# Kernel optimization log

Measured on AMD Instinct MI355X. Metric: run time of the kernel, lower is better.

The kernel has to match this reference:

```python
import jax, jax.numpy as jnp
import numpy as np

N_NODES = 100_000
N_EDGES = 1_600_000
HID = 64
LAYERS = 3
MAX_ATOM = 100
BATCH = 16


def setup_inputs() -> dict:
    key = jax.random.key(0)
    ks = jax.random.split(key, 24)
    s = 0.05  # weight scale
    inp = {
        "x": jax.random.normal(ks[0], (N_NODES, 3), dtype=jnp.float32),
        "z": jax.random.randint(ks[1], (N_NODES,), 0, MAX_ATOM),
        "t": jax.random.uniform(ks[2], (BATCH, 1), dtype=jnp.float32),
        "edge_index": jax.random.randint(ks[3], (2, N_EDGES), 0, N_NODES),
        # atom embedding table
        "emb": jax.random.normal(ks[4], (MAX_ATOM, HID)) * s,
        # time embedding MLP: Linear(1,H), SiLU, Linear(H,H)
        "t_w1": jax.random.normal(ks[5], (1, HID)) * s,
        "t_b1": jnp.zeros((HID,)),
        "t_w2": jax.random.normal(ks[6], (HID, HID)) * s,
        "t_b2": jnp.zeros((HID,)),
        # per-layer EGNN params, stacked over layers
        # edge MLP: Linear(2H+1, H), SiLU, Linear(H, H), SiLU
        "e_w1": jax.random.normal(ks[7], (LAYERS, 2 * HID + 1, HID)) * s,
        "e_b1": jnp.zeros((LAYERS, HID)),
        "e_w2": jax.random.normal(ks[8], (LAYERS, HID, HID)) * s,
        "e_b2": jnp.zeros((LAYERS, HID)),
        # coord MLP: Linear(H, H), SiLU, Linear(H, 1)
        "c_w1": jax.random.normal(ks[9], (LAYERS, HID, HID)) * s,
        "c_b1": jnp.zeros((LAYERS, HID)),
        "c_w2": jax.random.normal(ks[10], (LAYERS, HID, 1)) * s,
        "c_b2": jnp.zeros((LAYERS, 1)),
        # node MLP: Linear(2H, H), SiLU, Linear(H, H), residual
        "n_w1": jax.random.normal(ks[11], (LAYERS, 2 * HID, HID)) * s,
        "n_b1": jnp.zeros((LAYERS, HID)),
        "n_w2": jax.random.normal(ks[12], (LAYERS, HID, HID)) * s,
        "n_b2": jnp.zeros((LAYERS, HID)),
    }
    return inp


def reference(x, z, t, edge_index, emb,
              t_w1, t_b1, t_w2, t_b2,
              e_w1, e_b1, e_w2, e_b2,
              c_w1, c_b1, c_w2, c_b2,
              n_w1, n_b1, n_w2, n_b2):
    silu = jax.nn.silu
    n = x.shape[0]
    # atom embedding + global time conditioning
    h = emb[z]                                           # (N, H)
    t_emb = silu(t @ t_w1 + t_b1) @ t_w2 + t_b2          # (B, H)
    h = h + jnp.mean(t_emb, axis=0, keepdims=True)
    src, dst = edge_index[0], edge_index[1]
    for l in range(LAYERS):
        diff = x[dst] - x[src]                           # (E, 3)
        d2 = jnp.sum(diff * diff, axis=-1, keepdims=True)  # (E, 1)
        ef = jnp.concatenate([h[dst], h[src], d2], axis=-1)  # (E, 2H+1)
        m = silu(silu(ef @ e_w1[l] + e_b1[l]) @ e_w2[l] + e_b2[l])  # (E, H)
        cw = silu(m @ c_w1[l] + c_b1[l]) @ c_w2[l] + c_b2[l]        # (E, 1)
        x = x + jax.ops.segment_sum(diff * cw, dst, num_segments=n)
        agg = jax.ops.segment_sum(m, dst, num_segments=n)           # (N, H)
        nf = jnp.concatenate([h, agg], axis=-1)                     # (N, 2H)
        h = h + (silu(nf @ n_w1[l] + n_b1[l]) @ n_w2[l] + n_b2[l])
    return x
```

## Files before the change

kernel.cpp:

```cpp
#include <hip/hip_runtime.h>

typedef __attribute__((ext_vector_type(8))) short s8v;
typedef __attribute__((ext_vector_type(4))) float f32x4;

#define MFMA16(A,B,C) __builtin_amdgcn_mfma_f32_16x16x32_bf16((A),(B),(C),0,0,0)

__device__ __forceinline__ float b2f(unsigned short s){
  union { unsigned u; float f; } v; v.u = ((unsigned)s) << 16; return v.f;
}
__device__ __forceinline__ unsigned short f2b(float f){
  union { float f; unsigned u; } v; v.f = f;
  return (unsigned short)((v.u + 0x8000u) >> 16);
}
__device__ __forceinline__ float siluf(float x){
  return x * __builtin_amdgcn_rcpf(1.f + __expf(-x));
}


__global__ void hist_kernel(const int* __restrict__ dst, int* __restrict__ deg, int E){
  int i = blockIdx.x*256 + threadIdx.x;
  if (i < E) atomicAdd(&deg[dst[i]], 1);
}

__global__ void scan1_kernel(const int* __restrict__ deg, int* __restrict__ rp,
                             int* __restrict__ bsum, int N){
  __shared__ int s[256];
  const int base = blockIdx.x*1024;
  const int t = threadIdx.x;
  int v[4];
  #pragma unroll
  for (int j = 0; j < 4; ++j){
    int idx = base + t*4 + j;
    v[j] = (idx < N) ? deg[idx] : 0;
  }
  const int tsum = v[0]+v[1]+v[2]+v[3];
  s[t] = tsum;
  __syncthreads();
  for (int off = 1; off < 256; off <<= 1){
    int x = (t >= off) ? s[t-off] : 0;
    __syncthreads();
    s[t] += x;
    __syncthreads();
  }
  const int incl = s[t];
  if (t == 255) bsum[blockIdx.x] = incl;
  int run = incl - tsum;
  #pragma unroll
  for (int j = 0; j < 4; ++j){
    int idx = base + t*4 + j;
    if (idx < N) rp[idx] = run;
    run += v[j];
  }
}

__global__ void scan2_kernel(int* __restrict__ bsum, int nb){
  __shared__ int s[256];
  const int t = threadIdx.x;
  const int v = (t < nb) ? bsum[t] : 0;
  s[t] = v;
  __syncthreads();
  for (int off = 1; off < 256; off <<= 1){
    int x = (t >= off) ? s[t-off] : 0;
    __syncthreads();
    s[t] += x;
    __syncthreads();
  }
  if (t < nb) bsum[t] = s[t] - v;
}

__global__ void scan3_kernel(int* __restrict__ rp, const int* __restrict__ bsum,
                             int N, int E){
  int i = blockIdx.x*256 + threadIdx.x;
  if (i < N) rp[i] += bsum[i >> 10];
  if (i == 0) rp[N] = E;
}

__global__ void scatter_kernel(const int* __restrict__ src, const int* __restrict__ dst,
                               const int* __restrict__ rp, int* __restrict__ cursor,
                               int* __restrict__ csr_src, int E){
  int i = blockIdx.x*256 + threadIdx.x;
  if (i < E){
    const int d = dst[i];
    const int pos = rp[d] + atomicAdd(&cursor[d], 1);
    csr_src[pos] = src[i];
  }
}


__global__ void tmean_kernel(const float* __restrict__ t,
                             const float* __restrict__ tw1,
                             const float* __restrict__ tb1,
                             const float* __restrict__ tw2,
                             const float* __restrict__ tb2,
                             float* __restrict__ tmean){
  __shared__ __align__(16) float s1[16*64];
  int j = threadIdx.x;
  float w1 = tw1[j], bb1 = tb1[j];
  for (int b = 0; b < 16; ++b)
    s1[b*64 + j] = siluf(t[b] * w1 + bb1);
  __syncthreads();
  float acc = 0.f;
  for (int b = 0; b < 16; ++b)
    for (int k = 0; k < 64; ++k)
      acc += s1[b*64 + k] * tw2[k*64 + j];
  tmean[j] = tb2[j] + acc * (1.f/16.f);
}

__global__ void init_h_kernel(const int* __restrict__ z,
                              const float* __restrict__ emb,
                              const float* __restrict__ tmean,
                              float* __restrict__ hf,
                              unsigned short* __restrict__ hb, int N){
  int i = blockIdx.x*256 + threadIdx.x;
  if (i >= N*64) return;
  int j = i & 63;
  int n = i >> 6;
  float v = emb[z[n]*64 + j] + tmean[j];
  hf[i] = v;
  hb[i] = f2b(v);
}


__global__ __launch_bounds__(512) void p12_kernel(
    const unsigned short* __restrict__ hb,
    const float* __restrict__ ew1, const float* __restrict__ eb1,
    unsigned short* __restrict__ P1, unsigned short* __restrict__ P2,
    int layer, int N)
{
  __shared__ __align__(16) short w1a[64*72];
  __shared__ __align__(16) short w1b[64*72];
  __shared__ __align__(16) float b1s[64];

  const int tid = threadIdx.x;
  const float* w1g = ew1 + layer*129*64;
  for (int idx = tid; idx < 64*64; idx += 512){
    int k = idx >> 6, n = idx & 63;
    w1a[n*72 + k] = (short)f2b(w1g[k*64 + n]);
    w1b[n*72 + k] = (short)f2b(w1g[(64 + k)*64 + n]);
  }
  if (tid < 64) b1s[tid] = eb1[layer*64 + tid];
  __syncthreads();

  const int lane = tid & 63;
  const int wv = tid >> 6;
  const int q = lane >> 4;
  const int n16 = lane & 15;

  const int ntile = N >> 4;
  const int step = gridDim.x * 8;
  for (int t = blockIdx.x*8 + wv; t < ntile; t += step){
    const int row = t*16 + n16;
    const s8v* ph = (const s8v*)(hb + row*64);
    const s8v a0 = ph[q];
    const s8v a1 = ph[4+q];
    #pragma unroll
    for (int nt = 0; nt < 4; ++nt){
      const s8v* wa = (const s8v*)&w1a[(nt*16 + n16)*72];
      const s8v* wb = (const s8v*)&w1b[(nt*16 + n16)*72];
      f32x4 aA = {0.f,0.f,0.f,0.f};
      aA = MFMA16(a0, wa[q],   aA);
      aA = MFMA16(a1, wa[4+q], aA);
      f32x4 aB = {0.f,0.f,0.f,0.f};
      aB = MFMA16(a0, wb[q],   aB);
      aB = MFMA16(a1, wb[4+q], aB);
      const float bb = b1s[nt*16 + n16];
      #pragma unroll
      for (int r = 0; r < 4; ++r){
        const int o = (t*16 + q*4 + r)*64 + nt*16 + n16;
        P1[o] = f2b(aA[r] + bb);
        P2[o] = f2b(aB[r]);
      }
    }
  }
}


__global__ __launch_bounds__(512) void edge_csr_kernel(
    const int* __restrict__ rp, const int* __restrict__ csr_src,
    const float* __restrict__ x_in, float* __restrict__ x_out,
    const unsigned short* __restrict__ P1, const unsigned short* __restrict__ P2,
    unsigned short* __restrict__ aggb,
    const float* __restrict__ ew1,
    const float* __restrict__ ew2, const float* __restrict__ eb2,
    const float* __restrict__ cw1, const float* __restrict__ cb1,
    const float* __restrict__ cw2, const float* __restrict__ cb2,
    int layer, int do_agg, int N)
{
  __shared__ __align__(16) short wT2[64*72];
  __shared__ __align__(16) short wc1T[64*72];
  __shared__ __align__(16) short sc[8][16*72];
  __shared__ __align__(16) float sdiff[8][48];

  const int tid = threadIdx.x;
  const float* w2g = ew2 + layer*64*64;
  const float* c1g = cw1 + layer*64*64;
  for (int idx = tid; idx < 64*64; idx += 512){
    int k = idx >> 6, n = idx & 63;
    wT2[n*72 + k]  = (short)f2b(w2g[k*64 + n]);
    wc1T[n*72 + k] = (short)f2b(c1g[k*64 + n]);
  }

  const int lane = tid & 63;
  const int wv = tid >> 6;
  const int q = lane >> 4;
  const int n16 = lane & 15;
  short* mysc = sc[wv];
  float* mydiff = sdiff[wv];

  const float* wlg = ew1 + layer*129*64 + 128*64;
  float wl_lo[8], wl_hi[8];
  #pragma unroll
  for (int j = 0; j < 8; ++j){
    wl_lo[j] = wlg[q*8 + j];
    wl_hi[j] = wlg[32 + q*8 + j];
  }
  float be2r[4], bc1r[4], cw2r[4];
  #pragma unroll
  for (int nt = 0; nt < 4; ++nt){
    be2r[nt] = eb2[layer*64 + nt*16 + n16];
    bc1r[nt] = cb1[layer*64 + nt*16 + n16];
    cw2r[nt] = cw2[layer*64 + nt*16 + n16];
  }
  const float cb2s = cb2[layer];
  __syncthreads();

  const int nwave = gridDim.x * 8;
  for (int n = blockIdx.x*8 + wv; n < N; n += nwave){
    const int start = rp[n];
    const int deg = rp[n+1] - start;

    const s8v* pd = (const s8v*)(P1 + (size_t)n*64);
    const s8v lo1 = pd[q];
    const s8v hi1 = pd[4+q];
    const float xd0 = x_in[n*3+0];
    const float xd1 = x_in[n*3+1];
    const float xd2 = x_in[n*3+2];

    float colsum[4] = {0.f,0.f,0.f,0.f};
    float xacc0 = 0.f, xacc1 = 0.f, xacc2 = 0.f;

    const int nch = (deg + 15) >> 4;
    for (int c = 0; c < nch; ++c){
      const int row = c*16 + n16;
      const int si = (row < deg) ? csr_src[start + row] : n;
      const float xs0 = x_in[si*3+0];
      const float xs1 = x_in[si*3+1];
      const float xs2 = x_in[si*3+2];
      const float dx = xd0 - xs0;
      const float dy = xd1 - xs1;
      const float dz = xd2 - xs2;
      const float d2 = dx*dx + dy*dy + dz*dz;
      if (q == 0){ mydiff[n16*3+0]=dx; mydiff[n16*3+1]=dy; mydiff[n16*3+2]=dz; }

      const s8v* ps = (const s8v*)(P2 + (size_t)si*64);
      const s8v lo2 = ps[q];
      const s8v hi2 = ps[4+q];

      s8v alo, ahi;
      #pragma unroll
      for (int j = 0; j < 8; ++j){
        const float v0 = b2f((unsigned short)lo1[j]) + b2f((unsigned short)lo2[j]) + d2*wl_lo[j];
        alo[j] = (short)f2b(siluf(v0));
        const float v1 = b2f((unsigned short)hi1[j]) + b2f((unsigned short)hi2[j]) + d2*wl_hi[j];
        ahi[j] = (short)f2b(siluf(v1));
      }

      f32x4 acc2[4];
      #pragma unroll
      for (int nt = 0; nt < 4; ++nt){
        const s8v* wb = (const s8v*)&wT2[(nt*16 + n16)*72];
        f32x4 a = {0.f,0.f,0.f,0.f};
        a = MFMA16(alo, wb[q],   a);
        a = MFMA16(ahi, wb[4+q], a);
        acc2[nt] = a;
      }
      const int rowbase = c*16 + q*4;
      #pragma unroll
      for (int nt = 0; nt < 4; ++nt){
        const float bb = be2r[nt];
        #pragma unroll
        for (int r = 0; r < 4; ++r){
          const float mv = siluf(acc2[nt][r] + bb);
          mysc[(q*4 + r)*72 + nt*16 + n16] = (short)f2b(mv);
          colsum[nt] += (rowbase + r < deg) ? mv : 0.f;
        }
      }
      __builtin_amdgcn_wave_barrier();
      const s8v* srd = (const s8v*)&mysc[n16*72];
      const s8v m0 = srd[q];
      const s8v m1 = srd[4+q];
      __builtin_amdgcn_wave_barrier();

      float pr[4] = {0.f,0.f,0.f,0.f};
      #pragma unroll
      for (int nt = 0; nt < 4; ++nt){
        const s8v* wb = (const s8v*)&wc1T[(nt*16 + n16)*72];
        f32x4 a = {0.f,0.f,0.f,0.f};
        a = MFMA16(m0, wb[q],   a);
        a = MFMA16(m1, wb[4+q], a);
        const float bc = bc1r[nt];
        const float wc2 = cw2r[nt];
        #pragma unroll
        for (int r = 0; r < 4; ++r) pr[r] += siluf(a[r] + bc) * wc2;
      }
      #pragma unroll
      for (int off = 1; off < 16; off <<= 1){
        #pragma unroll
        for (int r = 0; r < 4; ++r) pr[r] += __shfl_xor(pr[r], off, 64);
      }
      #pragma unroll
      for (int r = 0; r < 4; ++r){
        const float cwv = pr[r] + cb2s;
        xacc0 += mydiff[(q*4 + r)*3 + 0] * cwv;
        xacc1 += mydiff[(q*4 + r)*3 + 1] * cwv;
        xacc2 += mydiff[(q*4 + r)*3 + 2] * cwv;
      }
    }

    #pragma unroll
    for (int nt = 0; nt < 4; ++nt){
      colsum[nt] += __shfl_xor(colsum[nt], 16, 64);
      colsum[nt] += __shfl_xor(colsum[nt], 32, 64);
    }
    xacc0 += __shfl_xor(xacc0, 16, 64); xacc0 += __shfl_xor(xacc0, 32, 64);
    xacc1 += __shfl_xor(xacc1, 16, 64); xacc1 += __shfl_xor(xacc1, 32, 64);
    xacc2 += __shfl_xor(xacc2, 16, 64); xacc2 += __shfl_xor(xacc2, 32, 64);

    if (do_agg && q == 0){
      #pragma unroll
      for (int nt = 0; nt < 4; ++nt)
        aggb[(size_t)n*64 + nt*16 + n16] = f2b(colsum[nt]);
    }
    if (lane == 0){
      x_out[n*3+0] = xd0 + xacc0;
      x_out[n*3+1] = xd1 + xacc1;
      x_out[n*3+2] = xd2 + xacc2;
    }
  }
}


__global__ __launch_bounds__(512) void node_p12_kernel(
    unsigned short* __restrict__ hb, float* __restrict__ hf,
    const unsigned short* __restrict__ aggb,
    const float* __restrict__ nw1, const float* __restrict__ nb1,
    const float* __restrict__ nw2, const float* __restrict__ nb2,
    const float* __restrict__ ew1, const float* __restrict__ eb1,
    unsigned short* __restrict__ P1, unsigned short* __restrict__ P2,
    int layer, int N)
{
  __shared__ __align__(16) short wT1[64*136];
  __shared__ __align__(16) short wT2[64*72];
  __shared__ __align__(16) short w1a[64*72];
  __shared__ __align__(16) short w1b[64*72];
  __shared__ __align__(16) short sc[8][16*72];
  __shared__ __align__(16) float b1s[64];
  __shared__ __align__(16) float b2s[64];
  __shared__ __align__(16) float eb1s[64];

  const int tid = threadIdx.x;
  const float* w1g = nw1 + layer*128*64;
  const float* w2g = nw2 + layer*64*64;
  const float* e1g = ew1 + (layer+1)*129*64;
  for (int idx = tid; idx < 64*128; idx += 512){
    int k = idx >> 6, n = idx & 63;
    wT1[n*136 + k] = (short)f2b(w1g[k*64 + n]);
  }
  for (int idx = tid; idx < 64*64; idx += 512){
    int k = idx >> 6, n = idx & 63;
    wT2[n*72 + k] = (short)f2b(w2g[k*64 + n]);
    w1a[n*72 + k] = (short)f2b(e1g[k*64 + n]);
    w1b[n*72 + k] = (short)f2b(e1g[(64 + k)*64 + n]);
  }
  if (tid < 64){
    b1s[tid]  = nb1[layer*64 + tid];
    b2s[tid]  = nb2[layer*64 + tid];
    eb1s[tid] = eb1[(layer+1)*64 + tid];
  }
  __syncthreads();

  const int lane = tid & 63;
  const int wv = tid >> 6;
  const int q = lane >> 4;
  const int n16 = lane & 15;
  short* mysc = sc[wv];

  const int ntile = N >> 4;
  const int step = gridDim.x * 8;
  for (int t = blockIdx.x*8 + wv; t < ntile; t += step){
    const int row = t*16 + n16;
    const s8v* ph = (const s8v*)(hb + row*64);
    const s8v a0 = ph[q];
    const s8v a1 = ph[4+q];
    const s8v* pa = (const s8v*)(aggb + (size_t)row*64);
    const s8v a2 = pa[q];
    const s8v a3 = pa[4+q];

    #pragma unroll
    for (int nt = 0; nt < 4; ++nt){
      const s8v* wb = (const s8v*)&wT1[(nt*16 + n16)*136];
      f32x4 a = {0.f,0.f,0.f,0.f};
      a = MFMA16(a0, wb[q],    a);
      a = MFMA16(a1, wb[4+q],  a);
      a = MFMA16(a2, wb[8+q],  a);
      a = MFMA16(a3, wb[12+q], a);
      const float bb = b1s[nt*16 + n16];
      #pragma unroll
      for (int r = 0; r < 4; ++r)
        mysc[(q*4 + r)*72 + nt*16 + n16] = (short)f2b(siluf(a[r] + bb));
    }
    __builtin_amdgcn_wave_barrier();
    const s8v* srd = (const s8v*)&mysc[n16*72];
    const s8v g0 = srd[q];
    const s8v g1 = srd[4+q];
    __builtin_amdgcn_wave_barrier();

    #pragma unroll
    for (int nt = 0; nt < 4; ++nt){
      const s8v* wb = (const s8v*)&wT2[(nt*16 + n16)*72];
      f32x4 a = {0.f,0.f,0.f,0.f};
      a = MFMA16(g0, wb[q],   a);
      a = MFMA16(g1, wb[4+q], a);
      const float bb = b2s[nt*16 + n16];
      #pragma unroll
      for (int r = 0; r < 4; ++r){
        const int idx = (t*16 + q*4 + r)*64 + nt*16 + n16;
        const float hv = hf[idx] + a[r] + bb;
        hf[idx] = hv;
        const unsigned short hvb = f2b(hv);
        hb[idx] = hvb;
        mysc[(q*4 + r)*72 + nt*16 + n16] = (short)hvb;
      }
    }
    __builtin_amdgcn_wave_barrier();
    const s8v h0 = srd[q];
    const s8v h1 = srd[4+q];
    __builtin_amdgcn_wave_barrier();

    #pragma unroll
    for (int nt = 0; nt < 4; ++nt){
      const s8v* wa = (const s8v*)&w1a[(nt*16 + n16)*72];
      const s8v* wb = (const s8v*)&w1b[(nt*16 + n16)*72];
      f32x4 aA = {0.f,0.f,0.f,0.f};
      aA = MFMA16(h0, wa[q],   aA);
      aA = MFMA16(h1, wa[4+q], aA);
      f32x4 aB = {0.f,0.f,0.f,0.f};
      aB = MFMA16(h0, wb[q],   aB);
      aB = MFMA16(h1, wb[4+q], aB);
      const float bb = eb1s[nt*16 + n16];
      #pragma unroll
      for (int r = 0; r < 4; ++r){
        const int o = (t*16 + q*4 + r)*64 + nt*16 + n16;
        P1[o] = f2b(aA[r] + bb);
        P2[o] = f2b(aB[r]);
      }
    }
  }
}


extern "C" void kernel_launch(void* const* d_in, const int* in_sizes, int n_in,
                              void* d_out, int out_size, void* d_ws, size_t ws_size,
                              hipStream_t stream)
{
  const float* x0   = (const float*)d_in[0];
  const int*   z    = (const int*)d_in[1];
  const float* tc   = (const float*)d_in[2];
  const int*   ei   = (const int*)d_in[3];
  const float* embc = (const float*)d_in[4];
  const float* tw1c = (const float*)d_in[5];
  const float* tb1c = (const float*)d_in[6];
  const float* tw2c = (const float*)d_in[7];
  const float* tb2c = (const float*)d_in[8];
  const float* ew1c = (const float*)d_in[9];
  const float* eb1c = (const float*)d_in[10];
  const float* ew2c = (const float*)d_in[11];
  const float* eb2c = (const float*)d_in[12];
  const float* cw1c = (const float*)d_in[13];
  const float* cb1c = (const float*)d_in[14];
  const float* cw2c = (const float*)d_in[15];
  const float* cb2c = (const float*)d_in[16];
  const float* nw1c = (const float*)d_in[17];
  const float* nb1c = (const float*)d_in[18];
  const float* nw2c = (const float*)d_in[19];
  const float* nb2c = (const float*)d_in[20];

  const int N = in_sizes[1];
  const int E = in_sizes[3] / 2;
  const int* srcp = ei;
  const int* dstp = ei + E;

  char* p = (char*)d_ws;
  auto alloc = [&](size_t bytes) -> void* {
    void* r = (void*)p; p += (bytes + 255) & ~(size_t)255; return r;
  };
  float* hf            = (float*)alloc((size_t)N*64*4);
  unsigned short* hbuf = (unsigned short*)alloc((size_t)N*64*2);
  unsigned short* aggb = (unsigned short*)alloc((size_t)N*64*2);
  unsigned short* P1   = (unsigned short*)alloc((size_t)N*64*2);
  unsigned short* P2   = (unsigned short*)alloc((size_t)N*64*2);
  float* xa            = (float*)alloc((size_t)N*3*4);
  float* xb            = (float*)alloc((size_t)N*3*4);
  float* tmean         = (float*)alloc(64*4);
  int*   degcur        = (int*)alloc((size_t)2*N*4);
  int*   deg           = degcur;
  int*   cursor        = degcur + N;
  int*   rowp          = (int*)alloc((size_t)(N+1)*4);
  int*   bsum          = (int*)alloc(256*4);
  int*   csr_src       = (int*)alloc((size_t)E*4);

  tmean_kernel<<<1, 64, 0, stream>>>(tc, tw1c, tb1c, tw2c, tb2c, tmean);
  init_h_kernel<<<(N*64 + 255)/256, 256, 0, stream>>>(z, embc, tmean, hf, hbuf, N);

  (void)hipMemsetAsync(degcur, 0, (size_t)2*N*4, stream);
  hist_kernel<<<(E + 255)/256, 256, 0, stream>>>(dstp, deg, E);
  const int nb = (N + 1023)/1024;
  scan1_kernel<<<nb, 256, 0, stream>>>(deg, rowp, bsum, N);
  scan2_kernel<<<1, 256, 0, stream>>>(bsum, nb);
  scan3_kernel<<<(N + 255)/256, 256, 0, stream>>>(rowp, bsum, N, E);
  scatter_kernel<<<(E + 255)/256, 256, 0, stream>>>(srcp, dstp, rowp, cursor, csr_src, E);

  p12_kernel<<<512, 512, 0, stream>>>(hbuf, ew1c, eb1c, P1, P2, 0, N);

  const float* xc = x0;
  float* xnexts[3] = {xa, xb, (float*)d_out};
  for (int l = 0; l < 3; ++l){
    float* xout = xnexts[l];
    edge_csr_kernel<<<1024, 512, 0, stream>>>(rowp, csr_src, xc, xout, P1, P2, aggb,
        ew1c, ew2c, eb2c, cw1c, cb1c, cw2c, cb2c, l, (l < 2) ? 1 : 0, N);
    if (l < 2)
      node_p12_kernel<<<512, 512, 0, stream>>>(hbuf, hf, aggb,
          nw1c, nb1c, nw2c, nb2c, ew1c, eb1c, P1, P2, l, N);
    xc = xout;
  }
}
```

Baseline: 933.0 us.

## Pack edges into 4-slot padded tiles and scatter-add aggregates atomically

Each node's degree is padded to a multiple of 4 and the CSR is regrouped into 16-edge tiles of four 4-edge slots, each slot tagged with its destination node. Waves now iterate over tiles rather than nodes, which removes the mostly-empty 16-row chunks that low-degree nodes left idle. Partial sums for messages and coordinate updates are merged across a pair of slots when they share a destination, then written with float atomics into an fp32 aggregate buffer. The cost is extra work per layer: a memset of the aggregate buffer, a copy of x, atomic contention, and an fp32 aggregate that the node kernel converts back to bf16.

```diff
diff --git a/kernel.cpp b/kernel.cpp
--- a/kernel.cpp
+++ b/kernel.cpp
@@ -31,7 +31,8 @@
   #pragma unroll
   for (int j = 0; j < 4; ++j){
     int idx = base + t*4 + j;
-    v[j] = (idx < N) ? deg[idx] : 0;
+    int dv = (idx < N) ? deg[idx] : 0;
+    v[j] = (dv + 3) & ~3;
   }
   const int tsum = v[0]+v[1]+v[2]+v[3];
   s[t] = tsum;
@@ -69,10 +70,13 @@
 }
 
 __global__ void scan3_kernel(int* __restrict__ rp, const int* __restrict__ bsum,
-                             int N, int E){
+                             const int* __restrict__ deg, int N){
   int i = blockIdx.x*256 + threadIdx.x;
-  if (i < N) rp[i] += bsum[i >> 10];
-  if (i == 0) rp[N] = E;
+  if (i < N){
+    int v = rp[i] + bsum[i >> 10];
+    rp[i] = v;
+    if (i == N-1) rp[N] = v + ((deg[i] + 3) & ~3);
+  }
 }
 
 __global__ void scatter_kernel(const int* __restrict__ src, const int* __restrict__ dst,
@@ -83,6 +87,31 @@
     const int d = dst[i];
     const int pos = rp[d] + atomicAdd(&cursor[d], 1);
     csr_src[pos] = src[i];
+  }
+}
+
+__global__ void slot_build_kernel(const int* __restrict__ rp, const int* __restrict__ deg,
+                                  int* __restrict__ slot_meta, int* __restrict__ csr_src,
+                                  int N){
+  int n = blockIdx.x*256 + threadIdx.x;
+  if (n < N){
+    const int base = rp[n];
+    const int d = deg[n];
+    const int ns = (d + 3) >> 2;
+    const int s0 = base >> 2;
+    for (int k = 0; k < ns; ++k){
+      int c = d - k*4; c = (c > 4) ? 4 : c;
+      slot_meta[s0 + k] = n | (c << 28);
+    }
+    for (int i = d; i < ns*4; ++i) csr_src[base + i] = n;
+  }
+  if (n == 0){
+    const int S  = rp[N] >> 2;
+    const int S4 = (S + 3) & ~3;
+    for (int s = S; s < S4; ++s){
+      slot_meta[s] = 0;
+      for (int r = 0; r < 4; ++r) csr_src[s*4 + r] = 0;
+    }
   }
 }
 
@@ -175,11 +204,12 @@
 }
 
 
-__global__ __launch_bounds__(512) void edge_csr_kernel(
+__global__ __launch_bounds__(512) void edge_tile_kernel(
     const int* __restrict__ rp, const int* __restrict__ csr_src,
+    const int* __restrict__ slot_meta,
     const float* __restrict__ x_in, float* __restrict__ x_out,
     const unsigned short* __restrict__ P1, const unsigned short* __restrict__ P2,
-    unsigned short* __restrict__ aggb,
+    float* __restrict__ aggf,
     const float* __restrict__ ew1,
     const float* __restrict__ ew2, const float* __restrict__ eb2,
     const float* __restrict__ cw1, const float* __restrict__ cb1,
@@ -224,117 +254,112 @@
   const float cb2s = cb2[layer];
   __syncthreads();
 
+  const int T = (rp[N] + 15) >> 4;
   const int nwave = gridDim.x * 8;
-  for (int n = blockIdx.x*8 + wv; n < N; n += nwave){
-    const int start = rp[n];
-    const int deg = rp[n+1] - start;
-
-    const s8v* pd = (const s8v*)(P1 + (size_t)n*64);
+  for (int t = blockIdx.x*8 + wv; t < T; t += nwave){
+    const int mi = slot_meta[t*4 + (n16 >> 2)];
+    const int di = mi & 0x0FFFFFFF;
+    const int si = csr_src[t*16 + n16];
+    const float dx = x_in[di*3+0] - x_in[si*3+0];
+    const float dy = x_in[di*3+1] - x_in[si*3+1];
+    const float dz = x_in[di*3+2] - x_in[si*3+2];
+    const float d2 = dx*dx + dy*dy + dz*dz;
+    if (q == 0){ mydiff[n16*3+0]=dx; mydiff[n16*3+1]=dy; mydiff[n16*3+2]=dz; }
+
+    const s8v* pd = (const s8v*)(P1 + (size_t)di*64);
     const s8v lo1 = pd[q];
     const s8v hi1 = pd[4+q];
-    const float xd0 = x_in[n*3+0];
-    const float xd1 = x_in[n*3+1];
-    const float xd2 = x_in[n*3+2];
+    const s8v* ps = (const s8v*)(P2 + (size_t)si*64);
+    const s8v lo2 = ps[q];
+    const s8v hi2 = ps[4+q];
+
+    s8v alo, ahi;
+    #pragma unroll
+    for (int j = 0; j < 8; ++j){
+      const float v0 = b2f((unsigned short)lo1[j]) + b2f((unsigned short)lo2[j]) + d2*wl_lo[j];
+      alo[j] = (short)f2b(siluf(v0));
+      const float v1 = b2f((unsigned short)hi1[j]) + b2f((unsigned short)hi2[j]) + d2*wl_hi[j];
+      ahi[j] = (short)f2b(siluf(v1));
+    }
+
+    f32x4 acc2[4];
+    #pragma unroll
+    for (int nt = 0; nt < 4; ++nt){
+      const s8v* wb = (const s8v*)&wT2[(nt*16 + n16)*72];
+      f32x4 a = {0.f,0.f,0.f,0.f};
+      a = MFMA16(alo, wb[q],   a);
+      a = MFMA16(ahi, wb[4+q], a);
+      acc2[nt] = a;
+    }
+
+    const int mo = slot_meta[t*4 + q];
+    const int dn = mo & 0x0FFFFFFF;
+    const int cnt = (int)(((unsigned)mo) >> 28);
 
     float colsum[4] = {0.f,0.f,0.f,0.f};
+    #pragma unroll
+    for (int nt = 0; nt < 4; ++nt){
+      const float bb = be2r[nt];
+      #pragma unroll
+      for (int r = 0; r < 4; ++r){
+        const float mv = siluf(acc2[nt][r] + bb);
+        mysc[(q*4 + r)*72 + nt*16 + n16] = (short)f2b(mv);
+        colsum[nt] += (r < cnt) ? mv : 0.f;
+      }
+    }
+    __builtin_amdgcn_wave_barrier();
+    const s8v* srd = (const s8v*)&mysc[n16*72];
+    const s8v m0 = srd[q];
+    const s8v m1 = srd[4+q];
+    __builtin_amdgcn_wave_barrier();
+
+    float pr[4] = {0.f,0.f,0.f,0.f};
+    #pragma unroll
+    for (int nt = 0; nt < 4; ++nt){
+      const s8v* wb = (const s8v*)&wc1T[(nt*16 + n16)*72];
+      f32x4 a = {0.f,0.f,0.f,0.f};
+      a = MFMA16(m0, wb[q],   a);
+      a = MFMA16(m1, wb[4+q], a);
+      const float bc = bc1r[nt];
+      const float wc2 = cw2r[nt];
+      #pragma unroll
+      for (int r = 0; r < 4; ++r) pr[r] += siluf(a[r] + bc) * wc2;
+    }
+    #pragma unroll
+    for (int off = 1; off < 16; off <<= 1){
+      #pragma unroll
+      for (int r = 0; r < 4; ++r) pr[r] += __shfl_xor(pr[r], off, 64);
+    }
     float xacc0 = 0.f, xacc1 = 0.f, xacc2 = 0.f;
-
-    const int nch = (deg + 15) >> 4;
-    for (int c = 0; c < nch; ++c){
-      const int row = c*16 + n16;
-      const int si = (row < deg) ? csr_src[start + row] : n;
-      const float xs0 = x_in[si*3+0];
-      const float xs1 = x_in[si*3+1];
-      const float xs2 = x_in[si*3+2];
-      const float dx = xd0 - xs0;
-      const float dy = xd1 - xs1;
-      const float dz = xd2 - xs2;
-      const float d2 = dx*dx + dy*dy + dz*dz;
-      if (q == 0){ mydiff[n16*3+0]=dx; mydiff[n16*3+1]=dy; mydiff[n16*3+2]=dz; }
-
-      const s8v* ps = (const s8v*)(P2 + (size_t)si*64);
-      const s8v lo2 = ps[q];
-      const s8v hi2 = ps[4+q];
-
-      s8v alo, ahi;
-      #pragma unroll
-      for (int j = 0; j < 8; ++j){
-        const float v0 = b2f((unsigned short)lo1[j]) + b2f((unsigned short)lo2[j]) + d2*wl_lo[j];
-        alo[j] = (short)f2b(siluf(v0));
-        const float v1 = b2f((unsigned short)hi1[j]) + b2f((unsigned short)hi2[j]) + d2*wl_hi[j];
-        ahi[j] = (short)f2b(siluf(v1));
-      }
-
-      f32x4 acc2[4];
-      #pragma unroll
-      for (int nt = 0; nt < 4; ++nt){
-        const s8v* wb = (const s8v*)&wT2[(nt*16 + n16)*72];
-        f32x4 a = {0.f,0.f,0.f,0.f};
-        a = MFMA16(alo, wb[q],   a);
-        a = MFMA16(ahi, wb[4+q], a);
-        acc2[nt] = a;
-      }
-      const int rowbase = c*16 + q*4;
-      #pragma unroll
-      for (int nt = 0; nt < 4; ++nt){
-        const float bb = be2r[nt];
-        #pragma unroll
-        for (int r = 0; r < 4; ++r){
-          const float mv = siluf(acc2[nt][r] + bb);
-          mysc[(q*4 + r)*72 + nt*16 + n16] = (short)f2b(mv);
-          colsum[nt] += (rowbase + r < deg) ? mv : 0.f;
-        }
-      }
-      __builtin_amdgcn_wave_barrier();
-      const s8v* srd = (const s8v*)&mysc[n16*72];
-      const s8v m0 = srd[q];
-      const s8v m1 = srd[4+q];
-      __builtin_amdgcn_wave_barrier();
-
-      float pr[4] = {0.f,0.f,0.f,0.f};
-      #pragma unroll
-      for (int nt = 0; nt < 4; ++nt){
-        const s8v* wb = (const s8v*)&wc1T[(nt*16 + n16)*72];
-        f32x4 a = {0.f,0.f,0.f,0.f};
-        a = MFMA16(m0, wb[q],   a);
-        a = MFMA16(m1, wb[4+q], a);
-        const float bc = bc1r[nt];
-        const float wc2 = cw2r[nt];
-        #pragma unroll
-        for (int r = 0; r < 4; ++r) pr[r] += siluf(a[r] + bc) * wc2;
-      }
-      #pragma unroll
-      for (int off = 1; off < 16; off <<= 1){
-        #pragma unroll
-        for (int r = 0; r < 4; ++r) pr[r] += __shfl_xor(pr[r], off, 64);
-      }
-      #pragma unroll
-      for (int r = 0; r < 4; ++r){
-        const float cwv = pr[r] + cb2s;
-        xacc0 += mydiff[(q*4 + r)*3 + 0] * cwv;
-        xacc1 += mydiff[(q*4 + r)*3 + 1] * cwv;
-        xacc2 += mydiff[(q*4 + r)*3 + 2] * cwv;
-      }
-    }
-
-    #pragma unroll
-    for (int nt = 0; nt < 4; ++nt){
-      colsum[nt] += __shfl_xor(colsum[nt], 16, 64);
-      colsum[nt] += __shfl_xor(colsum[nt], 32, 64);
-    }
-    xacc0 += __shfl_xor(xacc0, 16, 64); xacc0 += __shfl_xor(xacc0, 32, 64);
-    xacc1 += __shfl_xor(xacc1, 16, 64); xacc1 += __shfl_xor(xacc1, 32, 64);
-    xacc2 += __shfl_xor(xacc2, 16, 64); xacc2 += __shfl_xor(xacc2, 32, 64);
-
-    if (do_agg && q == 0){
+    #pragma unroll
+    for (int r = 0; r < 4; ++r){
+      const float cwv = pr[r] + cb2s;
+      xacc0 += mydiff[(q*4 + r)*3 + 0] * cwv;
+      xacc1 += mydiff[(q*4 + r)*3 + 1] * cwv;
+      xacc2 += mydiff[(q*4 + r)*3 + 2] * cwv;
+    }
+
+    const int dnb = __shfl_xor(dn, 16, 64);
+    const bool same = (dnb == dn);
+    #pragma unroll
+    for (int nt = 0; nt < 4; ++nt){
+      const float o = __shfl_xor(colsum[nt], 16, 64);
+      if (same) colsum[nt] += o;
+    }
+    const float o0 = __shfl_xor(xacc0, 16, 64);
+    const float o1 = __shfl_xor(xacc1, 16, 64);
+    const float o2 = __shfl_xor(xacc2, 16, 64);
+    if (same){ xacc0 += o0; xacc1 += o1; xacc2 += o2; }
+
+    const bool writer = ((q & 1) == 0) || !same;
+    if (do_agg && writer){
       #pragma unroll
       for (int nt = 0; nt < 4; ++nt)
-        aggb[(size_t)n*64 + nt*16 + n16] = f2b(colsum[nt]);
-    }
-    if (lane == 0){
-      x_out[n*3+0] = xd0 + xacc0;
-      x_out[n*3+1] = xd1 + xacc1;
-      x_out[n*3+2] = xd2 + xacc2;
+        atomicAdd(&aggf[(size_t)dn*64 + nt*16 + n16], colsum[nt]);
+    }
+    if (writer && n16 < 3){
+      const float v = (n16 == 0) ? xacc0 : (n16 == 1) ? xacc1 : xacc2;
+      atomicAdd(&x_out[dn*3 + n16], v);
     }
   }
 }
@@ -342,7 +367,7 @@
 
 __global__ __launch_bounds__(512) void node_p12_kernel(
     unsigned short* __restrict__ hb, float* __restrict__ hf,
-    const unsigned short* __restrict__ aggb,
+    const float* __restrict__ aggf,
     const float* __restrict__ nw1, const float* __restrict__ nb1,
     const float* __restrict__ nw2, const float* __restrict__ nb2,
     const float* __restrict__ ew1, const float* __restrict__ eb1,
@@ -392,9 +417,19 @@
     const s8v* ph = (const s8v*)(hb + row*64);
     const s8v a0 = ph[q];
     const s8v a1 = ph[4+q];
-    const s8v* pa = (const s8v*)(aggb + (size_t)row*64);
-    const s8v a2 = pa[q];
-    const s8v a3 = pa[4+q];
+    const f32x4* pa = (const f32x4*)(aggf + (size_t)row*64);
+    const f32x4 u0 = pa[2*q];
+    const f32x4 u1 = pa[2*q+1];
+    const f32x4 u2 = pa[8+2*q];
+    const f32x4 u3 = pa[9+2*q];
+    s8v a2, a3;
+    #pragma unroll
+    for (int j = 0; j < 4; ++j){
+      a2[j]   = (short)f2b(u0[j]);
+      a2[4+j] = (short)f2b(u1[j]);
+      a3[j]   = (short)f2b(u2[j]);
+      a3[4+j] = (short)f2b(u3[j]);
+    }
 
     #pragma unroll
     for (int nt = 0; nt < 4; ++nt){
@@ -496,7 +531,7 @@
   };
   float* hf            = (float*)alloc((size_t)N*64*4);
   unsigned short* hbuf = (unsigned short*)alloc((size_t)N*64*2);
-  unsigned short* aggb = (unsigned short*)alloc((size_t)N*64*2);
+  float* aggf          = (float*)alloc((size_t)N*64*4);
   unsigned short* P1   = (unsigned short*)alloc((size_t)N*64*2);
   unsigned short* P2   = (unsigned short*)alloc((size_t)N*64*2);
   float* xa            = (float*)alloc((size_t)N*3*4);
@@ -507,7 +542,8 @@
   int*   cursor        = degcur + N;
   int*   rowp          = (int*)alloc((size_t)(N+1)*4);
   int*   bsum          = (int*)alloc(256*4);
-  int*   csr_src       = (int*)alloc((size_t)E*4);
+  int*   csr_src       = (int*)alloc(((size_t)E + 3*(size_t)N + 64)*4);
+  int*   slot_meta     = (int*)alloc(((size_t)E/4 + (size_t)N + 16)*4);
 
   tmean_kernel<<<1, 64, 0, stream>>>(tc, tw1c, tb1c, tw2c, tb2c, tmean);
   init_h_kernel<<<(N*64 + 255)/256, 256, 0, stream>>>(z, embc, tmean, hf, hbuf, N);
@@ -517,8 +553,9 @@
   const int nb = (N + 1023)/1024;
   scan1_kernel<<<nb, 256, 0, stream>>>(deg, rowp, bsum, N);
   scan2_kernel<<<1, 256, 0, stream>>>(bsum, nb);
-  scan3_kernel<<<(N + 255)/256, 256, 0, stream>>>(rowp, bsum, N, E);
+  scan3_kernel<<<(N + 255)/256, 256, 0, stream>>>(rowp, bsum, deg, N);
   scatter_kernel<<<(E + 255)/256, 256, 0, stream>>>(srcp, dstp, rowp, cursor, csr_src, E);
+  slot_build_kernel<<<(N + 255)/256, 256, 0, stream>>>(rowp, deg, slot_meta, csr_src, N);
 
   p12_kernel<<<512, 512, 0, stream>>>(hbuf, ew1c, eb1c, P1, P2, 0, N);
 
@@ -526,10 +563,13 @@
   float* xnexts[3] = {xa, xb, (float*)d_out};
   for (int l = 0; l < 3; ++l){
     float* xout = xnexts[l];
-    edge_csr_kernel<<<1024, 512, 0, stream>>>(rowp, csr_src, xc, xout, P1, P2, aggb,
+    (void)hipMemcpyAsync(xout, xc, (size_t)N*3*4, hipMemcpyDeviceToDevice, stream);
+    if (l < 2) (void)hipMemsetAsync(aggf, 0, (size_t)N*64*4, stream);
+    edge_tile_kernel<<<1024, 512, 0, stream>>>(rowp, csr_src, slot_meta, xc, xout,
+        P1, P2, aggf,
         ew1c, ew2c, eb2c, cw1c, cb1c, cw2c, cb2c, l, (l < 2) ? 1 : 0, N);
     if (l < 2)
-      node_p12_kernel<<<512, 512, 0, stream>>>(hbuf, hf, aggb,
+      node_p12_kernel<<<512, 512, 0, stream>>>(hbuf, hf, aggf,
           nw1c, nb1c, nw2c, nb2c, ew1c, eb1c, P1, P2, l, N);
     xc = xout;
   }
```

New measurement: 826.2 us. -11.5%, faster.
